# Kernel optimization log

Measured on AMD Instinct MI355X. Metric: run time of the kernel, lower is better.

The kernel has to match this reference:

```python
import jax, jax.numpy as jnp
import numpy as np

N_NODES = 100000
N_EDGES = 1_600_000
D = 32


def setup_inputs() -> dict:
    key = jax.random.key(0)
    k1, k2, k3, k4, k5 = jax.random.split(key, 5)
    x = jax.random.normal(k1, (N_NODES, D), dtype=jnp.float32)
    W1 = jax.random.normal(k2, (D, D), dtype=jnp.float32) * (1.0 / np.sqrt(D))
    W2 = jax.random.normal(k3, (D, D), dtype=jnp.float32) * (1.0 / np.sqrt(D))
    b2 = jax.random.normal(k4, (D,), dtype=jnp.float32) * 0.01
    edge_index = jax.random.randint(k5, (2, N_EDGES), 0, N_NODES, dtype=jnp.int64)
    return {"x": x, "W1": W1, "W2": W2, "b2": b2, "edge_index": edge_index}


def reference(x, W1, W2, b2, edge_index):
    # ptensors0.transfer0 over the graph: F1[i] = sum_{(j->i) in E} x[j]
    src = edge_index[0]
    dst = edge_index[1]
    F1 = jax.ops.segment_sum(x[src], dst, num_segments=x.shape[0])  # [N, D]
    # out = lin2(x) + lin1(F1)  (lin2 has bias, lin1 does not; torch Linear: y = x @ W.T + b)
    return x @ W2.T + b2 + F1 @ W1.T
```

## Files before the change

### kernel.cpp

```cpp
#include <hip/hip_runtime.h>
#include <hip/hip_bf16.h>

#define DIM 32
#define LOG_NPB 7
#define NPB 128
#define CAP 4096
#define NBINS 800
#define EPB 4096
#define EPT 16

__global__ __launch_bounds__(256) void fused_lin_kernel(
    const float* __restrict__ x,
    const float* __restrict__ W1,
    const float* __restrict__ W2,
    const float* __restrict__ b2,
    float* __restrict__ out,
    unsigned* __restrict__ y32,
    int* __restrict__ cursor, int nb,
    int n_nodes)
{
    __shared__ float W1s[DIM][DIM];
    __shared__ float W2s[DIM][DIM];
    __shared__ float b2s[DIM];
    __shared__ float xs[8][DIM];

    const int t = threadIdx.x;

    if (blockIdx.x == 0) {
        for (int i = t; i < nb; i += 256) cursor[i] = i * CAP;
    }

    for (int i = t; i < DIM * DIM; i += 256) {
        int c = i >> 5, k = i & 31;
        W1s[k][c] = W1[i];
        W2s[k][c] = W2[i];
    }
    if (t < DIM) b2s[t] = b2[t];

    const int r = t >> 5;
    const int c = t & 31;
    const int ntiles = (n_nodes + 7) >> 3;

    for (int tile = blockIdx.x; tile < ntiles; tile += gridDim.x) {
        const int row = tile * 8 + r;
        __syncthreads();
        if (row < n_nodes) xs[r][c] = x[(long)row * DIM + c];
        __syncthreads();
        if (row < n_nodes) {
            float a2 = b2s[c];
            float a1 = 0.0f;
            #pragma unroll
            for (int k = 0; k < DIM; ++k) {
                float xv = xs[r][k];
                a2 += xv * W2s[k][c];
                a1 += xv * W1s[k][c];
            }
            out[(long)row * DIM + c] = a2;
            float hi = __shfl_down(a1, 1);
            if ((c & 1) == 0) {
                __hip_bfloat16 blo = __float2bfloat16(a1);
                __hip_bfloat16 bhi = __float2bfloat16(hi);
                unsigned pack = ((unsigned)(*(unsigned short*)&bhi) << 16)
                              | (unsigned)(*(unsigned short*)&blo);
                y32[(size_t)row * 16 + (c >> 1)] = pack;
            }
        }
    }
}

__global__ __launch_bounds__(256) void bucket_scatter_kernel(
    const int* __restrict__ src, const int* __restrict__ dst,
    int* __restrict__ cursor, unsigned* __restrict__ bedges, int nE)
{
    __shared__ int cnt[NBINS];
    __shared__ int base[NBINS];
    __shared__ int rank[NBINS];

    const int t = threadIdx.x;
    const long blockStart = (long)blockIdx.x * EPB;

    for (int i = t; i < NBINS; i += 256) { cnt[i] = 0; rank[i] = 0; }
    __syncthreads();

    int es[EPT], ed[EPT];
    #pragma unroll
    for (int i = 0; i < EPT; ++i) {
        long e = blockStart + i * 256 + t;
        if (e < nE) { es[i] = src[e]; ed[i] = dst[e]; }
        else        { es[i] = -1;     ed[i] = 0;      }
    }
    #pragma unroll
    for (int i = 0; i < EPT; ++i) {
        if (es[i] >= 0) atomicAdd(&cnt[ed[i] >> LOG_NPB], 1);
    }
    __syncthreads();

    for (int i = t; i < NBINS; i += 256) {
        int c = cnt[i];
        if (c > 0) base[i] = atomicAdd(&cursor[i], c);
    }
    __syncthreads();

    #pragma unroll
    for (int i = 0; i < EPT; ++i) {
        if (es[i] >= 0) {
            int b = ed[i] >> LOG_NPB;
            int r = atomicAdd(&rank[b], 1);
            int p = base[b] + r;
            if (p < (b + 1) * CAP)
                bedges[p] = ((unsigned)es[i] << LOG_NPB) | (unsigned)(ed[i] & (NPB - 1));
        }
    }
}

__global__ __launch_bounds__(512) void sort_gather_kernel(
    const int* __restrict__ cursor, const unsigned* __restrict__ bedges,
    const unsigned short* __restrict__ yb,
    float* __restrict__ out, int n_nodes)
{
    __shared__ unsigned ent[CAP];
    __shared__ unsigned sorted[CAP];
    __shared__ int cnt[NPB];
    __shared__ int ex[NPB];
    __shared__ int cur[NPB];

    const int b = blockIdx.x;
    const int t = threadIdx.x;
    const int start = b * CAP;
    int n = cursor[b] - start;
    if (n > CAP) n = CAP;
    if (n < 0) n = 0;

    if (t < NPB) { cnt[t] = 0; cur[t] = 0; }
    __syncthreads();

    for (int i = t; i < n; i += 512) {
        unsigned e = bedges[start + i];
        ent[i] = e;
        atomicAdd(&cnt[e & (NPB - 1)], 1);
    }
    __syncthreads();

    if (t < NPB) ex[t] = cnt[t];
    __syncthreads();
    for (int off = 1; off < NPB; off <<= 1) {
        int add = 0;
        if (t < NPB && t >= off) add = ex[t - off];
        __syncthreads();
        if (t < NPB) ex[t] += add;
        __syncthreads();
    }
    if (t < NPB) ex[t] -= cnt[t];
    __syncthreads();

    for (int i = t; i < n; i += 512) {
        unsigned e = ent[i];
        int bin = (int)(e & (NPB - 1));
        int r = atomicAdd(&cur[bin], 1);
        sorted[ex[bin] + r] = e >> LOG_NPB;
    }
    __syncthreads();

    const int wv   = t >> 6;
    const int lane = t & 63;
    const int slot = lane >> 3;
    const int li   = lane & 7;

    for (int ln = wv; ln < NPB; ln += 8) {
        const int node = b * NPB + ln;
        if (node >= n_nodes) break;
        const int st = ex[ln];
        const int d  = cnt[ln];
        if (d == 0) continue;

        float a0 = 0.f, a1 = 0.f, a2 = 0.f, a3 = 0.f;

        int s[4];
        #pragma unroll
        for (int k = 0; k < 4; ++k) {
            int e = slot + 8 * k;
            s[k] = (int)sorted[st + (e < d ? e : d - 1)];
        }
        ushort4 u[4];
        #pragma unroll
        for (int k = 0; k < 4; ++k)
            u[k] = *(const ushort4*)(yb + ((size_t)s[k] << 5) + (li << 2));
        #pragma unroll
        for (int k = 0; k < 4; ++k) {
            const bool v = (slot + 8 * k) < d;
            a0 += v ? __uint_as_float((unsigned)u[k].x << 16) : 0.f;
            a1 += v ? __uint_as_float((unsigned)u[k].y << 16) : 0.f;
            a2 += v ? __uint_as_float((unsigned)u[k].z << 16) : 0.f;
            a3 += v ? __uint_as_float((unsigned)u[k].w << 16) : 0.f;
        }

        for (int e0 = 32 + slot; e0 < d; e0 += 8) {
            int ss = (int)sorted[st + e0];
            ushort4 uu = *(const ushort4*)(yb + ((size_t)ss << 5) + (li << 2));
            a0 += __uint_as_float((unsigned)uu.x << 16);
            a1 += __uint_as_float((unsigned)uu.y << 16);
            a2 += __uint_as_float((unsigned)uu.z << 16);
            a3 += __uint_as_float((unsigned)uu.w << 16);
        }

        #pragma unroll
        for (int m = 8; m < 64; m <<= 1) {
            a0 += __shfl_xor(a0, m);
            a1 += __shfl_xor(a1, m);
            a2 += __shfl_xor(a2, m);
            a3 += __shfl_xor(a3, m);
        }

        if (slot == 0) {
            float4* orow = (float4*)(out + ((size_t)node << 5));
            float4 o = orow[li];
            o.x += a0; o.y += a1; o.z += a2; o.w += a3;
            orow[li] = o;
        }
    }
}

extern "C" void kernel_launch(void* const* d_in, const int* in_sizes, int n_in,
                              void* d_out, int out_size, void* d_ws, size_t ws_size,
                              hipStream_t stream) {
    const float* x  = (const float*)d_in[0];
    const float* W1 = (const float*)d_in[1];
    const float* W2 = (const float*)d_in[2];
    const float* b2 = (const float*)d_in[3];
    const int*   ei = (const int*)d_in[4];

    const int n_nodes = in_sizes[0] / DIM;
    const int n_edges = in_sizes[4] / 2;
    const int* src = ei;
    const int* dst = ei + n_edges;
    float* out = (float*)d_out;

    const int nb = (n_nodes + NPB - 1) / NPB;

    char* basep = (char*)d_ws;
    size_t off = 0;
    auto alloc = [&](size_t bytes) {
        char* p = basep + off;
        off = (off + bytes + 255) & ~(size_t)255;
        return p;
    };
    unsigned* y32    = (unsigned*)alloc((size_t)n_nodes * DIM * sizeof(unsigned short));
    int*      cursor = (int*)     alloc((size_t)nb * sizeof(int));
    unsigned* bedges = (unsigned*)alloc((size_t)nb * CAP * sizeof(unsigned));
    (void)ws_size;

    fused_lin_kernel<<<1024, 256, 0, stream>>>(x, W1, W2, b2, out, y32, cursor, nb, n_nodes);
    bucket_scatter_kernel<<<(n_edges + EPB - 1) / EPB, 256, 0, stream>>>(src, dst, cursor, bedges, n_edges);
    sort_gather_kernel<<<nb, 512, 0, stream>>>(cursor, bedges, (const unsigned short*)y32, out, n_nodes);
}
```

Measured before the change: 86.41 us.

## Move x@W2+b2 into gather kernel to drop out write-then-read round trip

Takes the W2 linear layer and bias out of the first kernel and computes them inside the sort/gather kernel. Each lane holds a 4x4 slice of W2 in registers and reduces x·W2 through the existing shuffle reduction. This removes one full write of out from the first kernel and the read-modify-write in the gather, so out is written once. In exchange the gather kernel reads x again and needs more registers for the W2 slice.

```diff
diff --git a/kernel.cpp b/kernel.cpp
--- a/kernel.cpp
+++ b/kernel.cpp
@@ -9,19 +9,14 @@
 #define EPB 4096
 #define EPT 16
 
-__global__ __launch_bounds__(256) void fused_lin_kernel(
+__global__ __launch_bounds__(256) void lin_y_kernel(
     const float* __restrict__ x,
     const float* __restrict__ W1,
-    const float* __restrict__ W2,
-    const float* __restrict__ b2,
-    float* __restrict__ out,
     unsigned* __restrict__ y32,
     int* __restrict__ cursor, int nb,
     int n_nodes)
 {
     __shared__ float W1s[DIM][DIM];
-    __shared__ float W2s[DIM][DIM];
-    __shared__ float b2s[DIM];
     __shared__ float xs[8][DIM];
 
     const int t = threadIdx.x;
@@ -33,9 +28,7 @@
     for (int i = t; i < DIM * DIM; i += 256) {
         int c = i >> 5, k = i & 31;
         W1s[k][c] = W1[i];
-        W2s[k][c] = W2[i];
-    }
-    if (t < DIM) b2s[t] = b2[t];
+    }
 
     const int r = t >> 5;
     const int c = t & 31;
@@ -47,15 +40,10 @@
         if (row < n_nodes) xs[r][c] = x[(long)row * DIM + c];
         __syncthreads();
         if (row < n_nodes) {
-            float a2 = b2s[c];
             float a1 = 0.0f;
             #pragma unroll
-            for (int k = 0; k < DIM; ++k) {
-                float xv = xs[r][k];
-                a2 += xv * W2s[k][c];
-                a1 += xv * W1s[k][c];
-            }
-            out[(long)row * DIM + c] = a2;
+            for (int k = 0; k < DIM; ++k)
+                a1 += xs[r][k] * W1s[k][c];
             float hi = __shfl_down(a1, 1);
             if ((c & 1) == 0) {
                 __hip_bfloat16 blo = __float2bfloat16(a1);
@@ -116,6 +104,9 @@
 __global__ __launch_bounds__(512) void sort_gather_kernel(
     const int* __restrict__ cursor, const unsigned* __restrict__ bedges,
     const unsigned short* __restrict__ yb,
+    const float* __restrict__ x,
+    const float* __restrict__ W2,
+    const float* __restrict__ b2,
     float* __restrict__ out, int n_nodes)
 {
     __shared__ unsigned ent[CAP];
@@ -126,6 +117,24 @@
 
     const int b = blockIdx.x;
     const int t = threadIdx.x;
+    const int wv   = t >> 6;
+    const int lane = t & 63;
+    const int slot = lane >> 3;
+    const int li   = lane & 7;
+
+    float w2t[4][4];
+    #pragma unroll
+    for (int j = 0; j < 4; ++j) {
+        #pragma unroll
+        for (int k = 0; k < 4; ++k)
+            w2t[k][j] = W2[(size_t)(4 * li + j) * DIM + 4 * slot + k];
+    }
+    float4 bias;
+    {
+        const float4* b4 = (const float4*)b2;
+        bias = b4[li];
+    }
+
     const int start = b * CAP;
     int n = cursor[b] - start;
     if (n > CAP) n = CAP;
@@ -161,46 +170,46 @@
     }
     __syncthreads();
 
-    const int wv   = t >> 6;
-    const int lane = t & 63;
-    const int slot = lane >> 3;
-    const int li   = lane & 7;
-
     for (int ln = wv; ln < NPB; ln += 8) {
         const int node = b * NPB + ln;
         if (node >= n_nodes) break;
         const int st = ex[ln];
         const int d  = cnt[ln];
-        if (d == 0) continue;
-
-        float a0 = 0.f, a1 = 0.f, a2 = 0.f, a3 = 0.f;
-
-        int s[4];
-        #pragma unroll
-        for (int k = 0; k < 4; ++k) {
-            int e = slot + 8 * k;
-            s[k] = (int)sorted[st + (e < d ? e : d - 1)];
-        }
-        ushort4 u[4];
-        #pragma unroll
-        for (int k = 0; k < 4; ++k)
-            u[k] = *(const ushort4*)(yb + ((size_t)s[k] << 5) + (li << 2));
-        #pragma unroll
-        for (int k = 0; k < 4; ++k) {
-            const bool v = (slot + 8 * k) < d;
-            a0 += v ? __uint_as_float((unsigned)u[k].x << 16) : 0.f;
-            a1 += v ? __uint_as_float((unsigned)u[k].y << 16) : 0.f;
-            a2 += v ? __uint_as_float((unsigned)u[k].z << 16) : 0.f;
-            a3 += v ? __uint_as_float((unsigned)u[k].w << 16) : 0.f;
-        }
-
-        for (int e0 = 32 + slot; e0 < d; e0 += 8) {
-            int ss = (int)sorted[st + e0];
-            ushort4 uu = *(const ushort4*)(yb + ((size_t)ss << 5) + (li << 2));
-            a0 += __uint_as_float((unsigned)uu.x << 16);
-            a1 += __uint_as_float((unsigned)uu.y << 16);
-            a2 += __uint_as_float((unsigned)uu.z << 16);
-            a3 += __uint_as_float((unsigned)uu.w << 16);
+
+        float4 xv = ((const float4*)(x + ((size_t)node << 5)))[slot];
+        float a0, a1, a2, a3;
+        a0 = xv.x * w2t[0][0] + xv.y * w2t[1][0] + xv.z * w2t[2][0] + xv.w * w2t[3][0];
+        a1 = xv.x * w2t[0][1] + xv.y * w2t[1][1] + xv.z * w2t[2][1] + xv.w * w2t[3][1];
+        a2 = xv.x * w2t[0][2] + xv.y * w2t[1][2] + xv.z * w2t[2][2] + xv.w * w2t[3][2];
+        a3 = xv.x * w2t[0][3] + xv.y * w2t[1][3] + xv.z * w2t[2][3] + xv.w * w2t[3][3];
+
+        if (d > 0) {
+            int s[4];
+            #pragma unroll
+            for (int k = 0; k < 4; ++k) {
+                int e = slot + 8 * k;
+                s[k] = (int)sorted[st + (e < d ? e : d - 1)];
+            }
+            ushort4 u[4];
+            #pragma unroll
+            for (int k = 0; k < 4; ++k)
+                u[k] = *(const ushort4*)(yb + ((size_t)s[k] << 5) + (li << 2));
+            #pragma unroll
+            for (int k = 0; k < 4; ++k) {
+                const bool v = (slot + 8 * k) < d;
+                a0 += v ? __uint_as_float((unsigned)u[k].x << 16) : 0.f;
+                a1 += v ? __uint_as_float((unsigned)u[k].y << 16) : 0.f;
+                a2 += v ? __uint_as_float((unsigned)u[k].z << 16) : 0.f;
+                a3 += v ? __uint_as_float((unsigned)u[k].w << 16) : 0.f;
+            }
+            for (int e0 = 32 + slot; e0 < d; e0 += 8) {
+                int ss = (int)sorted[st + e0];
+                ushort4 uu = *(const ushort4*)(yb + ((size_t)ss << 5) + (li << 2));
+                a0 += __uint_as_float((unsigned)uu.x << 16);
+                a1 += __uint_as_float((unsigned)uu.y << 16);
+                a2 += __uint_as_float((unsigned)uu.z << 16);
+                a3 += __uint_as_float((unsigned)uu.w << 16);
+            }
         }
 
         #pragma unroll
@@ -212,10 +221,12 @@
         }
 
         if (slot == 0) {
-            float4* orow = (float4*)(out + ((size_t)node << 5));
-            float4 o = orow[li];
-            o.x += a0; o.y += a1; o.z += a2; o.w += a3;
-            orow[li] = o;
+            float4 o;
+            o.x = a0 + bias.x;
+            o.y = a1 + bias.y;
+            o.z = a2 + bias.z;
+            o.w = a3 + bias.w;
+            ((float4*)(out + ((size_t)node << 5)))[li] = o;
         }
     }
 }
@@ -249,7 +260,8 @@
     unsigned* bedges = (unsigned*)alloc((size_t)nb * CAP * sizeof(unsigned));
     (void)ws_size;
 
-    fused_lin_kernel<<<1024, 256, 0, stream>>>(x, W1, W2, b2, out, y32, cursor, nb, n_nodes);
+    lin_y_kernel<<<1024, 256, 0, stream>>>(x, W1, y32, cursor, nb, n_nodes);
     bucket_scatter_kernel<<<(n_edges + EPB - 1) / EPB, 256, 0, stream>>>(src, dst, cursor, bedges, n_edges);
-    sort_gather_kernel<<<nb, 512, 0, stream>>>(cursor, bedges, (const unsigned short*)y32, out, n_nodes);
-}
+    sort_gather_kernel<<<nb, 512, 0, stream>>>(cursor, bedges, (const unsigned short*)y32,
+                                               x, W2, b2, out, n_nodes);
+}
```

After: 91.03 us. 5.3% more time.
